# Kernel tuning notes

Measured on AMD Instinct MI355X. Metric: run time of the kernel, lower is better.

Reference implementation:

```python
import jax, jax.numpy as jnp
import numpy as np

N = 4096
IN_SIZE = 512
MLP_W = 16
HID = 512
MID = 64  # hardcoded tgc2 output size in the torch module
OUT = 128
BN_EPS = 1e-5


def setup_inputs() -> dict:
    key = jax.random.key(0)
    ks = jax.random.split(key, 24)
    adj = (jax.random.uniform(ks[0], (N, N)) < 0.05).astype(jnp.float32)
    xdeg = jax.random.uniform(ks[1], (N, N), dtype=jnp.float32)
    ydeg = jax.random.uniform(ks[2], (N, N), dtype=jnp.float32)
    u = lambda k, sh, fan: jax.random.uniform(k, sh, jnp.float32, -1.0, 1.0) / np.sqrt(fan)
    return {
        "adj": adj, "xdeg": xdeg, "ydeg": ydeg,
        # edge MLP: 3 -> MLP_W -> 2
        "mlp_w1": u(ks[3], (3, MLP_W), 3), "mlp_b1": jnp.zeros((MLP_W,), jnp.float32),
        "mlp_w2": u(ks[4], (MLP_W, 2), MLP_W), "mlp_b2": jnp.zeros((2,), jnp.float32),
        # positional linear: Linear(N, in_size) applied to eye(N) -> pe = W^T + b
        "pe_w": u(ks[5], (N, IN_SIZE), N), "pe_b": jnp.zeros((IN_SIZE,), jnp.float32),
        # GCN weights
        "gc1_w": u(ks[6], (IN_SIZE, HID), HID),
        "lin2_w": u(ks[7], (HID, MID), HID), "lin2_b": jnp.zeros((MID,), jnp.float32),
        "gc3_w": u(ks[8], (MID, OUT), OUT),
        # BatchNorm (eval mode: running stats)
        "bn1_g": jnp.ones((HID,), jnp.float32), "bn1_b": jnp.zeros((HID,), jnp.float32),
        "bn1_m": jnp.zeros((HID,), jnp.float32), "bn1_v": jnp.ones((HID,), jnp.float32),
        "bn2_g": jnp.ones((OUT,), jnp.float32), "bn2_b": jnp.zeros((OUT,), jnp.float32),
        "bn2_m": jnp.zeros((OUT,), jnp.float32), "bn2_v": jnp.ones((OUT,), jnp.float32),
    }


def reference(adj, xdeg, ydeg, mlp_w1, mlp_b1, mlp_w2, mlp_b2, pe_w, pe_b,
              gc1_w, lin2_w, lin2_b, gc3_w,
              bn1_g, bn1_b, bn1_m, bn1_v, bn2_g, bn2_b, bn2_m, bn2_v):
    # Edge MLP + softmax over [adj, xdeg, ydeg] features; torch only computes it
    # at nonzero adj entries then scatters into a dense mask. Since the mask is
    # multiplied by adj, computing densely and multiplying is exactly equivalent.
    feats = jnp.stack([adj, xdeg, ydeg], axis=-1)          # [N, N, 3]
    h = jax.nn.relu(jnp.einsum('nmf,fw->nmw', feats, mlp_w1) + mlp_b1)
    logits = jnp.einsum('nmw,wc->nmc', h, mlp_w2) + mlp_b2  # [N, N, 2]
    mask = jax.nn.softmax(logits, axis=-1)[..., 1]          # [N, N]
    a = adj * mask + jnp.eye(adj.shape[0], dtype=adj.dtype)

    # Degree normalization: A' = D_row^{-1/2} A D_col^{-1/2} (broadcast, no diag matmuls)
    rowsum = jnp.sum(a, axis=1)
    colsum = jnp.sum(a, axis=0)
    d_row = jnp.where(rowsum > 0, rowsum ** -0.5, 0.0)
    d_col = jnp.where(colsum > 0, colsum ** -0.5, 0.0)
    a = d_row[:, None] * a * d_col[None, :]

    # pe = Linear(eye(N)) = W^T + b (eval mode, dropout off)
    pe = pe_w + pe_b[None, :]                               # [N, IN_SIZE]

    h = a @ (pe @ gc1_w)                                    # GCN layer 1
    h = (h - bn1_m) * (bn1_g / jnp.sqrt(bn1_v + BN_EPS)) + bn1_b
    h = h @ lin2_w + lin2_b                                 # tgc2
    mid = h
    h = jax.nn.relu(h)
    h = a @ (h @ gc3_w)                                     # GCN layer 3
    out = (h - bn2_m) * (bn2_g / jnp.sqrt(bn2_v + BN_EPS)) + bn2_b
    return out, mid
```

## Files before the change

kernel.cpp:

```cpp
#include <hip/hip_runtime.h>
#include <hip/hip_bf16.h>

#define NN 4096
#define INS 512
#define HIDW 512
#define MIDW 64
#define OUTW 128
#define CAP 384
#define BN_EPS 1e-5f
#define CS_BLOCKS 128
#define CS_ROWS (NN / CS_BLOCKS)

__global__ __launch_bounds__(256) void k_build(
    const float* __restrict__ adj, const float* __restrict__ xdeg,
    const float* __restrict__ ydeg,
    const float* __restrict__ w1, const float* __restrict__ b1,
    const float* __restrict__ w2, const float* __restrict__ b2,
    float* __restrict__ a_vals, int* __restrict__ a_cols, int* __restrict__ nnz,
    float* __restrict__ rowsum)
{
    __shared__ float shb[16], sw1x[16], sw1y[16], sw2[32], sb2[2];
    __shared__ int   scol[4][CAP];
    __shared__ float sx[4][CAP];
    __shared__ float sy[4][CAP];
    const int t = threadIdx.x;
    const int wave = t >> 6, lane = t & 63;
    const int i = blockIdx.x * 4 + wave;

    if (t < 16) {
        shb[t]  = b1[t] + w1[t];
        sw1x[t] = w1[16 + t];
        sw1y[t] = w1[32 + t];
    }
    if (t < 32) sw2[t] = w2[t];
    if (t < 2)  sb2[t] = b2[t];
    __syncthreads();

    const float* __restrict__ arow = adj  + (size_t)i * NN;
    const float* __restrict__ xrow = xdeg + (size_t)i * NN;
    const float* __restrict__ yrow = ydeg + (size_t)i * NN;
    const int j0 = 4 * lane;

    float4 a4 = *reinterpret_cast<const float4*>(arow + j0);
    float4 x4 = *reinterpret_cast<const float4*>(xrow + j0);
    float4 y4 = *reinterpret_cast<const float4*>(yrow + j0);

    int wbase = 0;
    bool has_diag_edge = false;
    for (int base = 0; base < NN; base += 256) {
        float4 an, xn, yn;
        if (base + 256 < NN) {
            an = *reinterpret_cast<const float4*>(arow + base + 256 + j0);
            xn = *reinterpret_cast<const float4*>(xrow + base + 256 + j0);
            yn = *reinterpret_cast<const float4*>(yrow + base + 256 + j0);
        }
        const float av[4] = {a4.x, a4.y, a4.z, a4.w};
        const float xv[4] = {x4.x, x4.y, x4.z, x4.w};
        const float yv[4] = {y4.x, y4.y, y4.z, y4.w};
        #pragma unroll
        for (int c = 0; c < 4; ++c) {
            int jj = base + j0 + c;
            bool nz = (av[c] != 0.f);
            bool active = nz || (jj == i);
            unsigned long long m  = __ballot(active);
            unsigned long long md = __ballot(nz && (jj == i));
            if (md) has_diag_edge = true;
            if (active) {
                int pos = wbase + __popcll(m & ((1ULL << lane) - 1));
                if (pos < CAP) {
                    scol[wave][pos] = jj;
                    sx[wave][pos]   = xv[c];
                    sy[wave][pos]   = yv[c];
                }
            }
            wbase += __popcll(m);
        }
        a4 = an; x4 = xn; y4 = yn;
    }
    const int n = (wbase < CAP) ? wbase : CAP;

    float local = 0.f;
    for (int p = lane; p < n; p += 64) {
        int jj = scol[wave][p];
        float v;
        if (jj == i && !has_diag_edge) {
            v = 1.f;
        } else {
            float x = sx[wave][p];
            float y = sy[wave][p];
            float l0 = sb2[0], l1 = sb2[1];
            #pragma unroll
            for (int w = 0; w < 16; ++w) {
                float hw = fmaf(x, sw1x[w], shb[w]);
                hw = fmaf(y, sw1y[w], hw);
                hw = fmaxf(hw, 0.f);
                l0 = fmaf(hw, sw2[2 * w],     l0);
                l1 = fmaf(hw, sw2[2 * w + 1], l1);
            }
            v = 1.f / (1.f + __expf(l0 - l1));
            if (jj == i) v += 1.f;
        }
        a_cols[(size_t)i * CAP + p] = jj;
        a_vals[(size_t)i * CAP + p] = v;
        local += v;
    }

    #pragma unroll
    for (int off = 32; off >= 1; off >>= 1)
        local += __shfl_down(local, off, 64);
    if (lane == 0) {
        nnz[i] = n;
        rowsum[i] = local;
    }
}

__global__ __launch_bounds__(256) void k_colsum(
    const float* __restrict__ a_vals, const int* __restrict__ a_cols,
    const int* __restrict__ nnz, float* __restrict__ P)
{
    __shared__ float ls[NN];
    const int t = threadIdx.x;
    const int b = blockIdx.x;
    for (int j = t; j < NN; j += 256) ls[j] = 0.f;
    __syncthreads();
    const int r0 = b * CS_ROWS;
    for (int r = r0; r < r0 + CS_ROWS; ++r) {
        const int n = nnz[r];
        const float* __restrict__ vr = a_vals + (size_t)r * CAP;
        const int*   __restrict__ cr = a_cols + (size_t)r * CAP;
        for (int p = t; p < n; p += 256)
            atomicAdd(&ls[cr[p]], vr[p]);
    }
    __syncthreads();
    for (int j = t; j < NN; j += 256)
        P[(size_t)b * NN + j] = ls[j];
}

__global__ __launch_bounds__(256) void k_scale2(
    const float* __restrict__ rowsum, const float* __restrict__ P,
    float* __restrict__ d_row, float* __restrict__ d_col)
{
    int j = blockIdx.x * 256 + threadIdx.x;
    float r = rowsum[j];
    d_row[j] = (r > 0.f) ? 1.f / sqrtf(r) : 0.f;
    float c = 0.f;
    for (int b = 0; b < CS_BLOCKS; ++b)
        c += P[(size_t)b * NN + j];
    d_col[j] = (c > 0.f) ? 1.f / sqrtf(c) : 0.f;
}

__global__ __launch_bounds__(512) void k_prep(
    const float* __restrict__ lin2_w, const float* __restrict__ lin2_b,
    const float* __restrict__ bn1_g, const float* __restrict__ bn1_b,
    const float* __restrict__ bn1_m, const float* __restrict__ bn1_v,
    const float* __restrict__ bn2_g, const float* __restrict__ bn2_b,
    const float* __restrict__ bn2_m, const float* __restrict__ bn2_v,
    float* __restrict__ Wp, float* __restrict__ c1,
    float* __restrict__ s2g, float* __restrict__ t2g)
{
    __shared__ float t1s[HIDW];
    const int t = threadIdx.x;
    {
        int h = t;
        float s1 = bn1_g[h] * rsqrtf(bn1_v[h] + BN_EPS);
        t1s[h] = bn1_b[h] - bn1_m[h] * s1;
        for (int m = 0; m < MIDW; ++m)
            Wp[(size_t)h * MIDW + m] = s1 * lin2_w[(size_t)h * MIDW + m];
    }
    __syncthreads();
    if (t < MIDW) {
        float acc = lin2_b[t];
        for (int h = 0; h < HIDW; ++h)
            acc = fmaf(t1s[h], lin2_w[(size_t)h * MIDW + t], acc);
        c1[t] = acc;
    } else if (t >= 64 && t < 64 + OUTW) {
        int j = t - 64;
        float s2 = bn2_g[j] * rsqrtf(bn2_v[j] + BN_EPS);
        s2g[j] = s2;
        t2g[j] = bn2_b[j] - bn2_m[j] * s2;
    }
}

template <bool ABIAS, bool ROWSCALE>
__global__ __launch_bounds__(256) void k_thin(
    const float* __restrict__ A, const float* __restrict__ B,
    const float* __restrict__ abias, const float* __restrict__ rscale,
    float* __restrict__ C, int M, int K)
{
    __shared__ float As[64][20];
    __shared__ float Bs[64][64];
    const int t = threadIdx.x;
    const int bm = blockIdx.x * 16;
    const int col = t & 63, rg = t >> 6;

    float acc[4] = {0.f, 0.f, 0.f, 0.f};

    for (int k0 = 0; k0 < K; k0 += 64) {
        #pragma unroll
        for (int l = 0; l < 4; ++l) {
            int e = t + l * 256;
            int r = e >> 6, k = e & 63;
            float v = A[(size_t)(bm + r) * K + k0 + k];
            if (ABIAS) v += abias[k0 + k];
            As[k][r] = v;
        }
        #pragma unroll
        for (int l = 0; l < 16; ++l) {
            int e = t + l * 256;
            int k = e >> 6, n = e & 63;
            Bs[k][n] = B[(size_t)(k0 + k) * 64 + n];
        }
        __syncthreads();
        #pragma unroll
        for (int k = 0; k < 64; ++k) {
            float4 a4 = *reinterpret_cast<const float4*>(&As[k][rg * 4]);
            float b = Bs[k][col];
            acc[0] = fmaf(a4.x, b, acc[0]);
            acc[1] = fmaf(a4.y, b, acc[1]);
            acc[2] = fmaf(a4.z, b, acc[2]);
            acc[3] = fmaf(a4.w, b, acc[3]);
        }
        __syncthreads();
    }

    #pragma unroll
    for (int u = 0; u < 4; ++u) {
        int r = bm + rg * 4 + u;
        float x = acc[u];
        if (ROWSCALE) x *= rscale[r];
        C[(size_t)r * 64 + col] = x;
    }
}

template <bool WITH_MID>
__global__ __launch_bounds__(64) void k_spmm64(
    const float* __restrict__ a_vals, const int* __restrict__ a_cols,
    const int* __restrict__ nnz, const float* __restrict__ X,
    const float* __restrict__ d_row, const float* __restrict__ d_col,
    const float* __restrict__ c1,
    float* __restrict__ O1, float* __restrict__ O2)
{
    __shared__ float sv[CAP];
    __shared__ int   scl[CAP];
    const int i = blockIdx.x;
    const int lane = threadIdx.x;
    const int n = nnz[i];
    const int n8 = (n + 7) & ~7;
    const float* __restrict__ vrow = a_vals + (size_t)i * CAP;
    const int*   __restrict__ crow = a_cols + (size_t)i * CAP;

    for (int p = lane; p < n8; p += 64) {
        bool ok = p < n;
        sv[p]  = ok ? vrow[p] : 0.f;
        scl[p] = ok ? crow[p] : 0;
    }
    __syncthreads();

    const int eh = lane >> 5;
    const int lc = lane & 31;
    const int npairs = n8 >> 1;

    float a0 = 0.f, a1 = 0.f;
    for (int q = 0; q < npairs; q += 4) {
        #pragma unroll
        for (int j = 0; j < 4; ++j) {
            int p = 2 * (q + j) + eh;
            float v = sv[p];
            int c = scl[p];
            float2 x = *reinterpret_cast<const float2*>(X + (size_t)c * 64 + 2 * lc);
            a0 = fmaf(v, x.x, a0);
            a1 = fmaf(v, x.y, a1);
        }
    }
    a0 += __shfl_xor(a0, 32);
    a1 += __shfl_xor(a1, 32);

    if (lane < 32) {
        float dr = d_row[i];
        if (WITH_MID) {
            float dc = d_col[i];
            float m0 = fmaf(a0, dr, c1[2 * lc]);
            float m1 = fmaf(a1, dr, c1[2 * lc + 1]);
            *reinterpret_cast<float2*>(O1 + (size_t)i * 64 + 2 * lc) =
                make_float2(m0, m1);
            *reinterpret_cast<float2*>(O2 + (size_t)i * 64 + 2 * lc) =
                make_float2(dc * fmaxf(m0, 0.f), dc * fmaxf(m1, 0.f));
        } else {
            *reinterpret_cast<float2*>(O1 + (size_t)i * 64 + 2 * lc) =
                make_float2(a0 * dr, a1 * dr);
        }
    }
}

__global__ __launch_bounds__(256) void k_out(
    const float* __restrict__ S, const float* __restrict__ gc3,
    const float* __restrict__ s2g, const float* __restrict__ t2g,
    float* __restrict__ out)
{
    __shared__ float Ss[64][20];
    __shared__ float Gs[64][128];
    const int t = threadIdx.x;
    const int bm = blockIdx.x * 16;

    {
        int r = t >> 4, c4 = (t & 15) * 4;
        float4 v = *reinterpret_cast<const float4*>(S + (size_t)(bm + r) * 64 + c4);
        Ss[c4 + 0][r] = v.x; Ss[c4 + 1][r] = v.y;
        Ss[c4 + 2][r] = v.z; Ss[c4 + 3][r] = v.w;
    }
    #pragma unroll
    for (int l = 0; l < 32; ++l) {
        int e = t + l * 256;
        Gs[e >> 7][e & 127] = gc3[e];
    }
    __syncthreads();

    const int j = t & 127;
    const int r0 = (t >> 7) * 8;
    float acc[8] = {};
    #pragma unroll
    for (int k = 0; k < 64; ++k) {
        float g = Gs[k][j];
        float4 a = *reinterpret_cast<const float4*>(&Ss[k][r0]);
        float4 b = *reinterpret_cast<const float4*>(&Ss[k][r0 + 4]);
        acc[0] = fmaf(a.x, g, acc[0]); acc[1] = fmaf(a.y, g, acc[1]);
        acc[2] = fmaf(a.z, g, acc[2]); acc[3] = fmaf(a.w, g, acc[3]);
        acc[4] = fmaf(b.x, g, acc[4]); acc[5] = fmaf(b.y, g, acc[5]);
        acc[6] = fmaf(b.z, g, acc[6]); acc[7] = fmaf(b.w, g, acc[7]);
    }
    float s2 = s2g[j], t2 = t2g[j];
    #pragma unroll
    for (int u = 0; u < 8; ++u)
        out[(size_t)(bm + r0 + u) * 128 + j] = fmaf(acc[u], s2, t2);
}

extern "C" void kernel_launch(void* const* d_in, const int* in_sizes, int n_in,
                              void* d_out, int out_size, void* d_ws, size_t ws_size,
                              hipStream_t stream) {
    const float* adj    = (const float*)d_in[0];
    const float* xdeg   = (const float*)d_in[1];
    const float* ydeg   = (const float*)d_in[2];
    const float* mlp_w1 = (const float*)d_in[3];
    const float* mlp_b1 = (const float*)d_in[4];
    const float* mlp_w2 = (const float*)d_in[5];
    const float* mlp_b2 = (const float*)d_in[6];
    const float* pe_w   = (const float*)d_in[7];
    const float* pe_b   = (const float*)d_in[8];
    const float* gc1_w  = (const float*)d_in[9];
    const float* lin2_w = (const float*)d_in[10];
    const float* lin2_b = (const float*)d_in[11];
    const float* gc3_w  = (const float*)d_in[12];
    const float* bn1_g  = (const float*)d_in[13];
    const float* bn1_b  = (const float*)d_in[14];
    const float* bn1_m  = (const float*)d_in[15];
    const float* bn1_v  = (const float*)d_in[16];
    const float* bn2_g  = (const float*)d_in[17];
    const float* bn2_b  = (const float*)d_in[18];
    const float* bn2_m  = (const float*)d_in[19];
    const float* bn2_v  = (const float*)d_in[20];

    float* out = (float*)d_out;
    float* mid = out + (size_t)NN * OUTW;

    char* w = (char*)d_ws;
    float* a_vals = (float*)w;  w += (size_t)NN * CAP * 4;
    int*   a_cols = (int*)w;    w += (size_t)NN * CAP * 4;
    int*   nnz    = (int*)w;    w += (size_t)NN * 4;
    float* rowsum = (float*)w;  w += (size_t)NN * 4;
    float* d_row  = (float*)w;  w += (size_t)NN * 4;
    float* d_col  = (float*)w;  w += (size_t)NN * 4;
    float* P      = (float*)w;  w += (size_t)CS_BLOCKS * NN * 4;
    float* Wp     = (float*)w;  w += (size_t)HIDW * MIDW * 4;
    float* W2     = (float*)w;  w += (size_t)INS * MIDW * 4;
    float* c1     = (float*)w;  w += 256;
    float* s2g    = (float*)w;  w += 512;
    float* t2g    = (float*)w;  w += 512;
    float* G      = (float*)w;  w += (size_t)NN * MIDW * 4;
    float* R      = (float*)w;  w += (size_t)NN * MIDW * 4;
    float* S      = (float*)w;  w += (size_t)NN * MIDW * 4;

    k_build<<<NN / 4, 256, 0, stream>>>(adj, xdeg, ydeg, mlp_w1, mlp_b1, mlp_w2,
                                        mlp_b2, a_vals, a_cols, nnz, rowsum);
    k_colsum<<<CS_BLOCKS, 256, 0, stream>>>(a_vals, a_cols, nnz, P);
    k_scale2<<<NN / 256, 256, 0, stream>>>(rowsum, P, d_row, d_col);
    k_prep<<<1, 512, 0, stream>>>(lin2_w, lin2_b, bn1_g, bn1_b, bn1_m, bn1_v,
                                  bn2_g, bn2_b, bn2_m, bn2_v, Wp, c1, s2g, t2g);
    k_thin<false, false><<<INS / 16, 256, 0, stream>>>(
        gc1_w, Wp, nullptr, nullptr, W2, INS, HIDW);
    k_thin<true, true><<<NN / 16, 256, 0, stream>>>(
        pe_w, W2, pe_b, d_col, G, NN, INS);
    k_spmm64<true><<<NN, 64, 0, stream>>>(
        a_vals, a_cols, nnz, G, d_row, d_col, c1, mid, R);
    k_spmm64<false><<<NN, 64, 0, stream>>>(
        a_vals, a_cols, nnz, R, d_row, d_col, nullptr, S, nullptr);
    k_out<<<NN / 16, 256, 0, stream>>>(S, gc3_w, s2g, t2g, out);
}
```

Measured before the change: 148.4 us.

## Split sparse adjacency build into count, prefix and parallel fill kernels

The single per-row build kernel, where one wave walked all 4096 columns in sequence, is replaced by three kernels. One builds per-strip ballot masks and counts from adj, one takes a per-row prefix over 16 strips, and one fills values and columns in parallel, with one wave per 256-column strip. The goal is far more memory-level parallelism on the dense xdeg/ydeg/adj streaming, which dominates cost. In exchange it adds two launches and small intermediate buffers, evaluates the edge MLP densely on every element, and reduces per-strip row sums in the scale kernel.

```diff
diff --git a/kernel.cpp b/kernel.cpp
--- a/kernel.cpp
+++ b/kernel.cpp
@@ -10,23 +10,63 @@
 #define BN_EPS 1e-5f
 #define CS_BLOCKS 128
 #define CS_ROWS (NN / CS_BLOCKS)
-
-__global__ __launch_bounds__(256) void k_build(
-    const float* __restrict__ adj, const float* __restrict__ xdeg,
-    const float* __restrict__ ydeg,
+#define NSTRIP 16
+
+__global__ __launch_bounds__(256) void k_count(
+    const float* __restrict__ adj,
+    unsigned long long* __restrict__ msk, int* __restrict__ cnt,
+    int* __restrict__ dflag)
+{
+    const int t = threadIdx.x;
+    const int wave = t >> 6, lane = t & 63;
+    const int gw = blockIdx.x * 4 + wave;
+    const int i = gw >> 4, s = gw & 15;
+    const int colbase = s * 256;
+    float4 a4 = *reinterpret_cast<const float4*>(
+        adj + (size_t)i * NN + colbase + 4 * lane);
+    const float av[4] = {a4.x, a4.y, a4.z, a4.w};
+    unsigned long long m[4];
+    int total = 0;
+    #pragma unroll
+    for (int c = 0; c < 4; ++c) {
+        int col = colbase + 4 * lane + c;
+        bool diag = (col == i);
+        bool act = (av[c] != 0.f) || diag;
+        if (diag) dflag[i] = (av[c] != 0.f) ? 1 : 0;
+        m[c] = __ballot(act);
+        total += __popcll(m[c]);
+    }
+    if (lane == 0) {
+        unsigned long long* mp = msk + (size_t)gw * 4;
+        mp[0] = m[0]; mp[1] = m[1]; mp[2] = m[2]; mp[3] = m[3];
+        cnt[gw] = total;
+    }
+}
+
+__global__ __launch_bounds__(256) void k_prefix(
+    const int* __restrict__ cnt, int* __restrict__ off, int* __restrict__ nnz)
+{
+    int i = blockIdx.x * 256 + threadIdx.x;
+    int run = 0;
+    #pragma unroll
+    for (int s = 0; s < NSTRIP; ++s) {
+        off[i * NSTRIP + s] = run;
+        run += cnt[i * NSTRIP + s];
+    }
+    nnz[i] = (run < CAP) ? run : CAP;
+}
+
+__global__ __launch_bounds__(256) void k_fill(
+    const float* __restrict__ xdeg, const float* __restrict__ ydeg,
+    const unsigned long long* __restrict__ msk, const int* __restrict__ off,
+    const int* __restrict__ dflag,
     const float* __restrict__ w1, const float* __restrict__ b1,
     const float* __restrict__ w2, const float* __restrict__ b2,
-    float* __restrict__ a_vals, int* __restrict__ a_cols, int* __restrict__ nnz,
-    float* __restrict__ rowsum)
+    float* __restrict__ a_vals, int* __restrict__ a_cols,
+    float* __restrict__ rs_part)
 {
     __shared__ float shb[16], sw1x[16], sw1y[16], sw2[32], sb2[2];
-    __shared__ int   scol[4][CAP];
-    __shared__ float sx[4][CAP];
-    __shared__ float sy[4][CAP];
-    const int t = threadIdx.x;
-    const int wave = t >> 6, lane = t & 63;
-    const int i = blockIdx.x * 4 + wave;
-
+    const int t = threadIdx.x;
     if (t < 16) {
         shb[t]  = b1[t] + w1[t];
         sw1x[t] = w1[16 + t];
@@ -36,82 +76,56 @@
     if (t < 2)  sb2[t] = b2[t];
     __syncthreads();
 
-    const float* __restrict__ arow = adj  + (size_t)i * NN;
-    const float* __restrict__ xrow = xdeg + (size_t)i * NN;
-    const float* __restrict__ yrow = ydeg + (size_t)i * NN;
-    const int j0 = 4 * lane;
-
-    float4 a4 = *reinterpret_cast<const float4*>(arow + j0);
-    float4 x4 = *reinterpret_cast<const float4*>(xrow + j0);
-    float4 y4 = *reinterpret_cast<const float4*>(yrow + j0);
-
-    int wbase = 0;
-    bool has_diag_edge = false;
-    for (int base = 0; base < NN; base += 256) {
-        float4 an, xn, yn;
-        if (base + 256 < NN) {
-            an = *reinterpret_cast<const float4*>(arow + base + 256 + j0);
-            xn = *reinterpret_cast<const float4*>(xrow + base + 256 + j0);
-            yn = *reinterpret_cast<const float4*>(yrow + base + 256 + j0);
-        }
-        const float av[4] = {a4.x, a4.y, a4.z, a4.w};
-        const float xv[4] = {x4.x, x4.y, x4.z, x4.w};
-        const float yv[4] = {y4.x, y4.y, y4.z, y4.w};
+    const int wave = t >> 6, lane = t & 63;
+    const int gw = blockIdx.x * 4 + wave;
+    const int i = gw >> 4, s = gw & 15;
+    const int colbase = s * 256;
+    const size_t rbase = (size_t)i * NN + colbase + 4 * lane;
+    float4 x4 = *reinterpret_cast<const float4*>(xdeg + rbase);
+    float4 y4 = *reinterpret_cast<const float4*>(ydeg + rbase);
+    const unsigned long long* mp = msk + (size_t)gw * 4;
+    unsigned long long m0 = mp[0], m1 = mp[1], m2 = mp[2], m3 = mp[3];
+    const int wb = off[gw];
+    const int hasde = dflag[i];
+
+    const unsigned long long ltmask = (1ULL << lane) - 1ULL;
+    int bases[4];
+    bases[0] = 0;
+    bases[1] = __popcll(m0);
+    bases[2] = bases[1] + __popcll(m1);
+    bases[3] = bases[2] + __popcll(m2);
+    const unsigned long long mm[4] = {m0, m1, m2, m3};
+
+    const float xv[4] = {x4.x, x4.y, x4.z, x4.w};
+    const float yv[4] = {y4.x, y4.y, y4.z, y4.w};
+    float* __restrict__ gv = a_vals + (size_t)i * CAP;
+    int*   __restrict__ gc = a_cols + (size_t)i * CAP;
+    float local = 0.f;
+    #pragma unroll
+    for (int c = 0; c < 4; ++c) {
+        bool act = (mm[c] >> lane) & 1ULL;
+        int col = colbase + 4 * lane + c;
+        float l0 = sb2[0], l1 = sb2[1];
         #pragma unroll
-        for (int c = 0; c < 4; ++c) {
-            int jj = base + j0 + c;
-            bool nz = (av[c] != 0.f);
-            bool active = nz || (jj == i);
-            unsigned long long m  = __ballot(active);
-            unsigned long long md = __ballot(nz && (jj == i));
-            if (md) has_diag_edge = true;
-            if (active) {
-                int pos = wbase + __popcll(m & ((1ULL << lane) - 1));
-                if (pos < CAP) {
-                    scol[wave][pos] = jj;
-                    sx[wave][pos]   = xv[c];
-                    sy[wave][pos]   = yv[c];
-                }
-            }
-            wbase += __popcll(m);
-        }
-        a4 = an; x4 = xn; y4 = yn;
-    }
-    const int n = (wbase < CAP) ? wbase : CAP;
-
-    float local = 0.f;
-    for (int p = lane; p < n; p += 64) {
-        int jj = scol[wave][p];
-        float v;
-        if (jj == i && !has_diag_edge) {
-            v = 1.f;
-        } else {
-            float x = sx[wave][p];
-            float y = sy[wave][p];
-            float l0 = sb2[0], l1 = sb2[1];
-            #pragma unroll
-            for (int w = 0; w < 16; ++w) {
-                float hw = fmaf(x, sw1x[w], shb[w]);
-                hw = fmaf(y, sw1y[w], hw);
-                hw = fmaxf(hw, 0.f);
-                l0 = fmaf(hw, sw2[2 * w],     l0);
-                l1 = fmaf(hw, sw2[2 * w + 1], l1);
-            }
-            v = 1.f / (1.f + __expf(l0 - l1));
-            if (jj == i) v += 1.f;
-        }
-        a_cols[(size_t)i * CAP + p] = jj;
-        a_vals[(size_t)i * CAP + p] = v;
-        local += v;
-    }
-
-    #pragma unroll
-    for (int off = 32; off >= 1; off >>= 1)
-        local += __shfl_down(local, off, 64);
-    if (lane == 0) {
-        nnz[i] = n;
-        rowsum[i] = local;
-    }
+        for (int w = 0; w < 16; ++w) {
+            float hw = fmaf(xv[c], sw1x[w], shb[w]);
+            hw = fmaf(yv[c], sw1y[w], hw);
+            hw = fmaxf(hw, 0.f);
+            l0 = fmaf(hw, sw2[2 * w],     l0);
+            l1 = fmaf(hw, sw2[2 * w + 1], l1);
+        }
+        float v = 1.f / (1.f + __expf(l0 - l1));
+        if (col == i) v = hasde ? (v + 1.f) : 1.f;
+        if (act) {
+            int pos = wb + bases[c] + __popcll(mm[c] & ltmask);
+            if (pos < CAP) { gc[pos] = col; gv[pos] = v; }
+            local += v;
+        }
+    }
+    #pragma unroll
+    for (int o = 32; o >= 1; o >>= 1)
+        local += __shfl_down(local, o, 64);
+    if (lane == 0) rs_part[gw] = local;
 }
 
 __global__ __launch_bounds__(256) void k_colsum(
@@ -137,11 +151,13 @@
 }
 
 __global__ __launch_bounds__(256) void k_scale2(
-    const float* __restrict__ rowsum, const float* __restrict__ P,
+    const float* __restrict__ rs_part, const float* __restrict__ P,
     float* __restrict__ d_row, float* __restrict__ d_col)
 {
     int j = blockIdx.x * 256 + threadIdx.x;
-    float r = rowsum[j];
+    float r = 0.f;
+    #pragma unroll
+    for (int s = 0; s < NSTRIP; ++s) r += rs_part[j * NSTRIP + s];
     d_row[j] = (r > 0.f) ? 1.f / sqrtf(r) : 0.f;
     float c = 0.f;
     for (int b = 0; b < CS_BLOCKS; ++b)
@@ -366,7 +382,11 @@
     float* a_vals = (float*)w;  w += (size_t)NN * CAP * 4;
     int*   a_cols = (int*)w;    w += (size_t)NN * CAP * 4;
     int*   nnz    = (int*)w;    w += (size_t)NN * 4;
-    float* rowsum = (float*)w;  w += (size_t)NN * 4;
+    unsigned long long* msk = (unsigned long long*)w; w += (size_t)NN * NSTRIP * 4 * 8;
+    int*   cnt    = (int*)w;    w += (size_t)NN * NSTRIP * 4;
+    int*   off    = (int*)w;    w += (size_t)NN * NSTRIP * 4;
+    int*   dflag  = (int*)w;    w += (size_t)NN * 4;
+    float* rs_part= (float*)w;  w += (size_t)NN * NSTRIP * 4;
     float* d_row  = (float*)w;  w += (size_t)NN * 4;
     float* d_col  = (float*)w;  w += (size_t)NN * 4;
     float* P      = (float*)w;  w += (size_t)CS_BLOCKS * NN * 4;
@@ -379,10 +399,13 @@
     float* R      = (float*)w;  w += (size_t)NN * MIDW * 4;
     float* S      = (float*)w;  w += (size_t)NN * MIDW * 4;
 
-    k_build<<<NN / 4, 256, 0, stream>>>(adj, xdeg, ydeg, mlp_w1, mlp_b1, mlp_w2,
-                                        mlp_b2, a_vals, a_cols, nnz, rowsum);
+    k_count<<<NN * NSTRIP / 4, 256, 0, stream>>>(adj, msk, cnt, dflag);
+    k_prefix<<<NN / 256, 256, 0, stream>>>(cnt, off, nnz);
+    k_fill<<<NN * NSTRIP / 4, 256, 0, stream>>>(
+        xdeg, ydeg, msk, off, dflag, mlp_w1, mlp_b1, mlp_w2, mlp_b2,
+        a_vals, a_cols, rs_part);
     k_colsum<<<CS_BLOCKS, 256, 0, stream>>>(a_vals, a_cols, nnz, P);
-    k_scale2<<<NN / 256, 256, 0, stream>>>(rowsum, P, d_row, d_col);
+    k_scale2<<<NN / 256, 256, 0, stream>>>(rs_part, P, d_row, d_col);
     k_prep<<<1, 512, 0, stream>>>(lin2_w, lin2_b, bn1_g, bn1_b, bn1_m, bn1_v,
                                   bn2_g, bn2_b, bn2_m, bn2_v, Wp, c1, s2g, t2g);
     k_thin<false, false><<<INS / 16, 256, 0, stream>>>(
```

After: 188.4 us. 27.0% more time.
